# Optimization experiments

Measured on AMD Instinct MI355X. Metric: run time of the kernel, lower is better.

The kernel has to match this reference:

```python
import jax, jax.numpy as jnp
import numpy as np

B, F, V, D_EMB = 16384, 32, 50000, 16
D_IN = F * D_EMB            # 512, concat embedding dim
N_TASK, N_SPEC, N_SH = 2, 2, 2
E = N_TASK * N_SPEC + N_SH  # 6 experts per CGC level
H1, H2 = 512, 256           # expert_params dims
T1, T2 = 128, 64            # tower dims


def setup_inputs() -> dict:
    key = jax.random.key(0)
    ks = iter(jax.random.split(key, 32))
    def w(shape, s=0.05):
        return jax.random.normal(next(ks), shape, jnp.float32) * s
    return dict(
        x_ids=jax.random.randint(next(ks), (B, F), 0, V),
        emb=w((F, V, D_EMB)),
        e1_W1=w((E, D_IN, H1)), e1_b1=jnp.zeros((E, H1), jnp.float32),
        e1_W2=w((E, H1, H2)), e1_b2=jnp.zeros((E, H2), jnp.float32),
        g1_Ws=w((N_TASK, D_IN, N_SPEC + N_SH)), g1_bs=jnp.zeros((N_TASK, N_SPEC + N_SH), jnp.float32),
        g1_Wsh=w((D_IN, E)), g1_bsh=jnp.zeros((E,), jnp.float32),
        e2_W1=w((E, H2, H1)), e2_b1=jnp.zeros((E, H1), jnp.float32),
        e2_W2=w((E, H1, H2)), e2_b2=jnp.zeros((E, H2), jnp.float32),
        g2_Ws=w((N_TASK, H2, N_SPEC + N_SH)), g2_bs=jnp.zeros((N_TASK, N_SPEC + N_SH), jnp.float32),
        tw_W1=w((N_TASK, H2, T1)), tw_b1=jnp.zeros((N_TASK, T1), jnp.float32),
        tw_W2=w((N_TASK, T1, T2)), tw_b2=jnp.zeros((N_TASK, T2), jnp.float32),
    )


def _cgc(x_list, W1, b1, W2, b2, Wg, bg, Wg_sh=None, bg_sh=None):
    # Stack expert inputs: task-t specific experts read x_list[t], shared read x_list[-1].
    X = jnp.stack([x_list[0]] * N_SPEC + [x_list[1]] * N_SPEC + [x_list[-1]] * N_SH)  # [E,B,Din]
    # Grouped two-layer expert MLP (BatchNorm is identity at eval-mode init).
    h = jax.nn.relu(jnp.einsum('ebd,edh->ebh', X, W1) + b1[:, None, :])   # [E,B,H1]
    out = jax.nn.relu(jnp.einsum('ebh,eho->ebo', h, W2) + b2[:, None, :])  # [E,B,H2]
    outs = []
    for t in range(N_TASK):
        gate = jax.nn.softmax(x_list[t] @ Wg[t] + bg[t], axis=-1)          # [B, N_SPEC+N_SH]
        sel = jnp.concatenate([out[t * N_SPEC:(t + 1) * N_SPEC], out[-N_SH:]], axis=0)
        outs.append(jnp.einsum('bk,kbo->bo', gate, sel))
    if Wg_sh is not None:  # shared gate only for levels < n_level
        gate = jax.nn.softmax(x_list[-1] @ Wg_sh + bg_sh, axis=-1)          # [B,E]
        outs.append(jnp.einsum('bk,kbo->bo', gate, out))
    return outs


def reference(x_ids, emb, e1_W1, e1_b1, e1_W2, e1_b2, g1_Ws, g1_bs, g1_Wsh, g1_bsh,
              e2_W1, e2_b1, e2_W2, e2_b2, g2_Ws, g2_bs, tw_W1, tw_b1, tw_W2, tw_b2):
    # Embedding lookup per sparse feature, then flatten (squeeze_dim=True).
    embed_x = emb[jnp.arange(F)[None, :], x_ids].reshape(B, D_IN)  # [B, 512]
    xs = [embed_x] * (N_TASK + 1)
    xs = _cgc(xs, e1_W1, e1_b1, e1_W2, e1_b2, g1_Ws, g1_bs, g1_Wsh, g1_bsh)  # level 1 -> 3 outs
    xs = _cgc(xs, e2_W1, e2_b1, e2_W2, e2_b2, g2_Ws, g2_bs)                  # level 2 -> 2 outs
    ys = []
    for t in range(N_TASK):
        h = jax.nn.relu(xs[t] @ tw_W1[t] + tw_b1[t])
        h = jax.nn.relu(h @ tw_W2[t] + tw_b2[t])
        ys.append(jax.nn.sigmoid(h))  # PredictionLayer('classification')
    return jnp.concatenate(ys, axis=1)  # [B, N_TASK*T2]
```

## Files before the change

### kernel.cpp

```cpp
#include <hip/hip_runtime.h>

typedef unsigned short u16;
typedef __attribute__((ext_vector_type(4))) unsigned short u16x4;
typedef __attribute__((ext_vector_type(8))) unsigned short u16x8;
typedef __attribute__((ext_vector_type(8))) short s16x8;
typedef __attribute__((ext_vector_type(4))) float f32x4;

#define BATCH 16384
#define NFEAT 32
#define NVOCAB 50000

__device__ __forceinline__ u16 f2bf(float f) {
    union { float f; unsigned u; } v; v.f = f;
    unsigned u = v.u;
    return (u16)((u + 0x7fffu + ((u >> 16) & 1u)) >> 16);
}
__device__ __forceinline__ float bf2f(u16 h) {
    union { unsigned u; float f; } v; v.u = ((unsigned)h) << 16;
    return v.f;
}

__device__ __forceinline__ void load_lds16(const u16* g, u16* l) {
    __builtin_amdgcn_global_load_lds(
        (const __attribute__((address_space(1))) void*)g,
        (__attribute__((address_space(3))) void*)l, 16, 0, 0);
}

struct PrepDesc { const float* src; u16* dst; int K; int N; int nz; int zbase; };
struct PrepArgs { PrepDesc d[6]; };

__global__ void prep_weights(PrepArgs args) {
    int z = blockIdx.z;
    int di = 0;
    #pragma unroll
    for (int i = 0; i < 6; i++)
        if (z >= args.d[i].zbase && z < args.d[i].zbase + args.d[i].nz) di = i;
    PrepDesc d = args.d[di];
    int zz = z - d.zbase;
    int k0 = blockIdx.x * 32, n0 = blockIdx.y * 32;
    if (k0 >= d.K || n0 >= d.N) return;
    __shared__ float tile[32][33];
    const float* src = d.src + (long)zz * d.K * d.N;
    u16* dst = d.dst + (long)zz * d.K * d.N;
    int tx = threadIdx.x & 31, ty = threadIdx.x >> 5;
    for (int r = ty; r < 32; r += 8) {
        int k = k0 + r, n = n0 + tx;
        tile[r][tx] = (k < d.K && n < d.N) ? src[(long)k * d.N + n] : 0.f;
    }
    __syncthreads();
    for (int r = ty; r < 32; r += 8) {
        int n = n0 + r, k = k0 + tx;
        if (n < d.N && k < d.K) dst[(long)n * d.K + k] = f2bf(tile[tx][r]);
    }
}

__global__ void gather_embed(const int* __restrict__ ids,
                             const float* __restrict__ emb,
                             u16* __restrict__ out) {
    int idx = blockIdx.x * 256 + threadIdx.x;
    int d4 = idx & 3;
    int f  = (idx >> 2) & 31;
    int b  = idx >> 7;
    int id = ids[b * NFEAT + f];
    const float4* p = (const float4*)(emb + ((long)f * NVOCAB + id) * 16) + d4;
    float4 v = *p;
    u16x4 o;
    o.x = f2bf(v.x); o.y = f2bf(v.y); o.z = f2bf(v.z); o.w = f2bf(v.w);
    *(u16x4*)(out + (long)b * 512 + f * 16 + d4 * 4) = o;
}

struct FusedP {
    const u16* A; const u16* W1t; const float* b1;
    const u16* W2t; const float* b2; u16* O;
    int K1, a_zshift; long a_zstride;
};

__device__ __forceinline__ void expert_impl(const FusedP p) {
    __shared__ u16 sA[64 * 64];
    __shared__ u16 sW[256 * 64];
    __shared__ u16 sH[64 * 128];
    const int z = blockIdx.z;
    const int m0 = blockIdx.x * 64;
    const u16* Ab  = p.A + (long)(z >> p.a_zshift) * p.a_zstride;
    const u16* W1b = p.W1t + (long)z * 512 * p.K1;
    const u16* W2b = p.W2t + (long)z * 256 * 512;
    const int K1 = p.K1;
    const int tid = threadIdx.x;
    const int lane = tid & 63;
    const int w = tid >> 6;
    const int l16 = lane & 15;
    const int q = lane >> 4;
    const int key = l16 & 7;

    const int tr = tid >> 3;
    const int lc = (tid & 7) ^ (tr & 7);
    const u16* gA0 = Ab + (long)(m0 + tr) * K1 + lc * 8;
    const int ldst = (tid & ~63) * 8;

    f32x4 acc[4][4] = {};

    #pragma unroll
    for (int c = 0; c < 4; c++) {
        f32x4 acc1[4][2] = {};
        for (int k0 = 0; k0 < K1; k0 += 64) {
            __syncthreads();
            #pragma unroll
            for (int i = 0; i < 2; i++)
                load_lds16(gA0 + (long)(32 * i) * K1 + k0, &sA[i * 2048 + ldst]);
            #pragma unroll
            for (int i = 0; i < 4; i++)
                load_lds16(W1b + (long)(c * 128 + 32 * i + tr) * K1 + k0 + lc * 8,
                           &sW[i * 2048 + ldst]);
            __syncthreads();
            #pragma unroll
            for (int kk = 0; kk < 2; kk++) {
                const int pc = ((kk << 2) | q) ^ key;
                s16x8 af[4], bf[2];
                #pragma unroll
                for (int mt = 0; mt < 4; mt++)
                    af[mt] = *(const s16x8*)(&sA[(mt * 16 + l16) * 64 + pc * 8]);
                #pragma unroll
                for (int nt = 0; nt < 2; nt++)
                    bf[nt] = *(const s16x8*)(&sW[(w * 32 + nt * 16 + l16) * 64 + pc * 8]);
                #pragma unroll
                for (int mt = 0; mt < 4; mt++)
                    #pragma unroll
                    for (int nt = 0; nt < 2; nt++)
                        acc1[mt][nt] = __builtin_amdgcn_mfma_f32_16x16x32_bf16(
                            bf[nt], af[mt], acc1[mt][nt], 0, 0, 0);
            }
        }
        __syncthreads();
        {
            const float* bb1 = p.b1 + (long)z * 512 + c * 128;
            #pragma unroll
            for (int mt = 0; mt < 4; mt++) {
                int r = mt * 16 + l16;
                #pragma unroll
                for (int nt = 0; nt < 2; nt++) {
                    int col = w * 32 + nt * 16 + q * 4;
                    float4 bv = *(const float4*)(bb1 + col);
                    f32x4 v = acc1[mt][nt];
                    u16x4 o;
                    o.x = f2bf(fmaxf(v.x + bv.x, 0.f));
                    o.y = f2bf(fmaxf(v.y + bv.y, 0.f));
                    o.z = f2bf(fmaxf(v.z + bv.z, 0.f));
                    o.w = f2bf(fmaxf(v.w + bv.w, 0.f));
                    int c8 = col >> 3;
                    *(u16x4*)(&sH[r * 128 + ((c8 ^ (r & 7)) << 3) + (q & 1) * 4]) = o;
                }
            }
        }
        #pragma unroll
        for (int s = 0; s < 2; s++) {
            __syncthreads();
            #pragma unroll
            for (int i = 0; i < 8; i++)
                load_lds16(W2b + (long)(32 * i + tr) * 512 + c * 128 + s * 64 + lc * 8,
                           &sW[i * 2048 + ldst]);
            __syncthreads();
            #pragma unroll
            for (int kk = 0; kk < 2; kk++) {
                const int kg = s * 8 + ((kk << 2) | q);
                const int pc = ((kk << 2) | q) ^ key;
                s16x8 af[4], bf[4];
                #pragma unroll
                for (int mt = 0; mt < 4; mt++) {
                    int r = mt * 16 + l16;
                    af[mt] = *(const s16x8*)(&sH[r * 128 + ((kg ^ key) << 3)]);
                }
                #pragma unroll
                for (int nt = 0; nt < 4; nt++)
                    bf[nt] = *(const s16x8*)(&sW[(w * 64 + nt * 16 + l16) * 64 + pc * 8]);
                #pragma unroll
                for (int mt = 0; mt < 4; mt++)
                    #pragma unroll
                    for (int nt = 0; nt < 4; nt++)
                        acc[mt][nt] = __builtin_amdgcn_mfma_f32_16x16x32_bf16(
                            bf[nt], af[mt], acc[mt][nt], 0, 0, 0);
            }
        }
    }

    const float* bb2 = p.b2 + (long)z * 256;
    u16* Op = p.O + (long)z * BATCH * 256;
    #pragma unroll
    for (int mt = 0; mt < 4; mt++) {
        int grow = m0 + mt * 16 + l16;
        u16* rowp = Op + (long)grow * 256;
        #pragma unroll
        for (int nt = 0; nt < 4; nt++) {
            int gc = w * 64 + nt * 16 + q * 4;
            float4 bv = *(const float4*)(bb2 + gc);
            f32x4 v = acc[mt][nt];
            v.x = fmaxf(v.x + bv.x, 0.f);
            v.y = fmaxf(v.y + bv.y, 0.f);
            v.z = fmaxf(v.z + bv.z, 0.f);
            v.w = fmaxf(v.w + bv.w, 0.f);
            u16x4 o;
            o.x = f2bf(v.x); o.y = f2bf(v.y); o.z = f2bf(v.z); o.w = f2bf(v.w);
            *(u16x4*)(rowp + gc) = o;
        }
    }
}

__global__ __launch_bounds__(256, 2) void fused_l1(FusedP p) { expert_impl(p); }
__global__ __launch_bounds__(256, 2) void fused_l2(FusedP p) { expert_impl(p); }

__global__ __launch_bounds__(256, 1)
void tower_fused(const u16* __restrict__ x2, const u16* __restrict__ W1t,
                 const float* __restrict__ b1, const u16* __restrict__ W2t,
                 const float* __restrict__ b2, float* __restrict__ out) {
    const int t = blockIdx.y, m0 = blockIdx.x * 64;
    __shared__ u16 sX[64 * 256];
    __shared__ u16 sW1[128 * 256];
    __shared__ u16 sH[64 * 136];
    __shared__ u16 sW2[64 * 128];
    __shared__ float sB1[128];
    __shared__ float sB2[64];
    const int tid = threadIdx.x, lane = tid & 63, w = tid >> 6;
    const int l16 = lane & 15, q = lane >> 4;

    #pragma unroll
    for (int i = 0; i < 8; i++) {
        int c = i * 256 + tid, row = c >> 5, kc = c & 31;
        int lcc = (kc & ~7) | ((kc & 7) ^ (row & 7));
        load_lds16(x2 + ((long)t * BATCH + m0 + row) * 256 + lcc * 8,
                   &sX[(i * 256 + (tid & ~63)) * 8]);
    }
    #pragma unroll
    for (int i = 0; i < 16; i++) {
        int c = i * 256 + tid, row = c >> 5, kc = c & 31;
        int lcc = (kc & ~7) | ((kc & 7) ^ (row & 7));
        load_lds16(W1t + ((long)t * 128 + row) * 256 + lcc * 8,
                   &sW1[(i * 256 + (tid & ~63)) * 8]);
    }
    #pragma unroll
    for (int i = 0; i < 4; i++) {
        int c = i * 256 + tid, row = c >> 4, kc = c & 15;
        int lcc = (kc & ~7) | ((kc & 7) ^ (row & 7));
        load_lds16(W2t + ((long)t * 64 + row) * 128 + lcc * 8,
                   &sW2[(i * 256 + (tid & ~63)) * 8]);
    }
    if (tid < 128) sB1[tid] = b1[t * 128 + tid];
    if (tid < 64)  sB2[tid] = b2[t * 64 + tid];
    __syncthreads();

    f32x4 acc1[4][2] = {};
    #pragma unroll
    for (int kk = 0; kk < 8; kk++) {
        int pcb = kk * 4 + q;
        s16x8 af[4], bf[2];
        #pragma unroll
        for (int mt = 0; mt < 4; mt++) {
            int row = mt * 16 + l16;
            int sc = (pcb & ~7) | ((pcb & 7) ^ (row & 7));
            af[mt] = *(const s16x8*)(&sX[row * 256 + sc * 8]);
        }
        #pragma unroll
        for (int nt = 0; nt < 2; nt++) {
            int row = w * 32 + nt * 16 + l16;
            int sc = (pcb & ~7) | ((pcb & 7) ^ (row & 7));
            bf[nt] = *(const s16x8*)(&sW1[row * 256 + sc * 8]);
        }
        #pragma unroll
        for (int mt = 0; mt < 4; mt++)
            #pragma unroll
            for (int nt = 0; nt < 2; nt++)
                acc1[mt][nt] = __builtin_amdgcn_mfma_f32_16x16x32_bf16(
                    bf[nt], af[mt], acc1[mt][nt], 0, 0, 0);
    }
    #pragma unroll
    for (int mt = 0; mt < 4; mt++) {
        int row = mt * 16 + l16;
        #pragma unroll
        for (int nt = 0; nt < 2; nt++) {
            int col = w * 32 + nt * 16 + q * 4;
            f32x4 v = acc1[mt][nt];
            u16x4 o;
            o.x = f2bf(fmaxf(v.x + sB1[col + 0], 0.f));
            o.y = f2bf(fmaxf(v.y + sB1[col + 1], 0.f));
            o.z = f2bf(fmaxf(v.z + sB1[col + 2], 0.f));
            o.w = f2bf(fmaxf(v.w + sB1[col + 3], 0.f));
            *(u16x4*)(&sH[row * 136 + col]) = o;
        }
    }
    __syncthreads();

    f32x4 acc2[4] = {};
    #pragma unroll
    for (int kk = 0; kk < 4; kk++) {
        s16x8 af[4], bf;
        #pragma unroll
        for (int mt = 0; mt < 4; mt++) {
            int row = mt * 16 + l16;
            af[mt] = *(const s16x8*)(&sH[row * 136 + kk * 32 + q * 8]);
        }
        {
            int row = w * 16 + l16;
            int pc = kk * 4 + q;
            int sc = (pc & ~7) | ((pc & 7) ^ (row & 7));
            bf = *(const s16x8*)(&sW2[row * 128 + sc * 8]);
        }
        #pragma unroll
        for (int mt = 0; mt < 4; mt++)
            acc2[mt] = __builtin_amdgcn_mfma_f32_16x16x32_bf16(
                bf, af[mt], acc2[mt], 0, 0, 0);
    }
    #pragma unroll
    for (int mt = 0; mt < 4; mt++) {
        int grow = m0 + mt * 16 + l16;
        int col = w * 16 + q * 4;
        float4 bv = *(const float4*)(sB2 + col);
        f32x4 v = acc2[mt];
        float4 r;
        r.x = 1.f / (1.f + __expf(-(v.x + bv.x)));
        r.y = 1.f / (1.f + __expf(-(v.y + bv.y)));
        r.z = 1.f / (1.f + __expf(-(v.z + bv.z)));
        r.w = 1.f / (1.f + __expf(-(v.w + bv.w)));
        *(float4*)(out + (long)grow * 128 + t * 64 + col) = r;
    }
}

__global__ __launch_bounds__(256)
void gate1(const u16* __restrict__ embed, const u16* __restrict__ out1,
           const float* __restrict__ g1Ws, const float* __restrict__ g1bs,
           const float* __restrict__ gWsh, const float* __restrict__ gbsh,
           u16* __restrict__ x1) {
    const int m0 = blockIdx.x * 8;
    __shared__ float sg[8][16];
    const int tid = threadIdx.x;
    const int row = tid >> 5, l = tid & 31;
    const long rb = m0 + row;

    float a[4] = {0,0,0,0}, b[4] = {0,0,0,0}, c[6] = {0,0,0,0,0,0};
    {
        const u16* er = embed + rb * 512 + l * 16;
        u16x8 xa = *(const u16x8*)(er);
        u16x8 xb = *(const u16x8*)(er + 8);
        #pragma unroll
        for (int u = 0; u < 16; u++) {
            int k = l * 16 + u;
            float xv = bf2f(u < 8 ? xa[u] : xb[u - 8]);
            float4 wa = *(const float4*)(g1Ws + k * 4);
            float4 wb = *(const float4*)(g1Ws + 2048 + k * 4);
            a[0] += xv * wa.x; a[1] += xv * wa.y; a[2] += xv * wa.z; a[3] += xv * wa.w;
            b[0] += xv * wb.x; b[1] += xv * wb.y; b[2] += xv * wb.z; b[3] += xv * wb.w;
            float2 w0 = *(const float2*)(gWsh + k * 6);
            float2 w1 = *(const float2*)(gWsh + k * 6 + 2);
            float2 w2 = *(const float2*)(gWsh + k * 6 + 4);
            c[0] += xv * w0.x; c[1] += xv * w0.y;
            c[2] += xv * w1.x; c[3] += xv * w1.y;
            c[4] += xv * w2.x; c[5] += xv * w2.y;
        }
    }
    #pragma unroll
    for (int off = 1; off < 32; off <<= 1) {
        #pragma unroll
        for (int g = 0; g < 4; g++) { a[g] += __shfl_xor(a[g], off); b[g] += __shfl_xor(b[g], off); }
        #pragma unroll
        for (int g = 0; g < 6; g++) c[g] += __shfl_xor(c[g], off);
    }
    if (l == 0) {
        float mx, s, e[6];
        mx = -1e30f;
        for (int g = 0; g < 4; g++) { a[g] += g1bs[g]; mx = fmaxf(mx, a[g]); }
        s = 0.f; for (int g = 0; g < 4; g++) { e[g] = __expf(a[g] - mx); s += e[g]; }
        for (int g = 0; g < 4; g++) sg[row][g] = e[g] / s;
        mx = -1e30f;
        for (int g = 0; g < 4; g++) { b[g] += g1bs[4 + g]; mx = fmaxf(mx, b[g]); }
        s = 0.f; for (int g = 0; g < 4; g++) { e[g] = __expf(b[g] - mx); s += e[g]; }
        for (int g = 0; g < 4; g++) sg[row][4 + g] = e[g] / s;
        mx = -1e30f;
        for (int g = 0; g < 6; g++) { c[g] += gbsh[g]; mx = fmaxf(mx, c[g]); }
        s = 0.f; for (int g = 0; g < 6; g++) { e[g] = __expf(c[g] - mx); s += e[g]; }
        for (int g = 0; g < 6; g++) sg[row][8 + g] = e[g] / s;
    }
    __syncthreads();

    const int c8 = l * 8;
    const u16* ob = out1 + rb * 256 + c8;
    u16x8 o[6];
    #pragma unroll
    for (int k = 0; k < 6; k++) o[k] = *(const u16x8*)(ob + (long)k * BATCH * 256);
    const float* g = sg[row];
    u16x8 r0, r1, r2;
    #pragma unroll
    for (int u = 0; u < 8; u++) {
        float o0 = bf2f(o[0][u]), o1 = bf2f(o[1][u]), o2 = bf2f(o[2][u]);
        float o3 = bf2f(o[3][u]), o4 = bf2f(o[4][u]), o5 = bf2f(o[5][u]);
        r0[u] = f2bf(g[0] * o0 + g[1] * o1 + g[2] * o4 + g[3] * o5);
        r1[u] = f2bf(g[4] * o2 + g[5] * o3 + g[6] * o4 + g[7] * o5);
        r2[u] = f2bf(g[8] * o0 + g[9] * o1 + g[10] * o2 + g[11] * o3 + g[12] * o4 + g[13] * o5);
    }
    *(u16x8*)(x1 + ((long)0 * BATCH + rb) * 256 + c8) = r0;
    *(u16x8*)(x1 + ((long)1 * BATCH + rb) * 256 + c8) = r1;
    *(u16x8*)(x1 + ((long)2 * BATCH + rb) * 256 + c8) = r2;
}

__global__ __launch_bounds__(256)
void gate2(const u16* __restrict__ x1, const u16* __restrict__ out2,
           const float* __restrict__ g2Ws, const float* __restrict__ g2bs,
           u16* __restrict__ x2) {
    const int m0 = blockIdx.x * 8;
    __shared__ float sg[8][8];
    const int tid = threadIdx.x;
    const int row = tid >> 5, l = tid & 31;
    const long rb = m0 + row;

    float a[4] = {0,0,0,0}, b[4] = {0,0,0,0};
    {
        const u16* e0 = x1 + rb * 256 + l * 8;
        const u16* e1 = e0 + (long)BATCH * 256;
        u16x8 x0 = *(const u16x8*)e0;
        u16x8 x1v = *(const u16x8*)e1;
        #pragma unroll
        for (int u = 0; u < 8; u++) {
            int k = l * 8 + u;
            float4 wa = *(const float4*)(g2Ws + k * 4);
            float4 wb = *(const float4*)(g2Ws + 1024 + k * 4);
            float xv0 = bf2f(x0[u]), xv1 = bf2f(x1v[u]);
            a[0] += xv0 * wa.x; a[1] += xv0 * wa.y; a[2] += xv0 * wa.z; a[3] += xv0 * wa.w;
            b[0] += xv1 * wb.x; b[1] += xv1 * wb.y; b[2] += xv1 * wb.z; b[3] += xv1 * wb.w;
        }
    }
    #pragma unroll
    for (int off = 1; off < 32; off <<= 1) {
        #pragma unroll
        for (int g = 0; g < 4; g++) { a[g] += __shfl_xor(a[g], off); b[g] += __shfl_xor(b[g], off); }
    }
    if (l == 0) {
        float mx, s, e[4];
        mx = -1e30f;
        for (int g = 0; g < 4; g++) { a[g] += g2bs[g]; mx = fmaxf(mx, a[g]); }
        s = 0.f; for (int g = 0; g < 4; g++) { e[g] = __expf(a[g] - mx); s += e[g]; }
        for (int g = 0; g < 4; g++) sg[row][g] = e[g] / s;
        mx = -1e30f;
        for (int g = 0; g < 4; g++) { b[g] += g2bs[4 + g]; mx = fmaxf(mx, b[g]); }
        s = 0.f; for (int g = 0; g < 4; g++) { e[g] = __expf(b[g] - mx); s += e[g]; }
        for (int g = 0; g < 4; g++) sg[row][4 + g] = e[g] / s;
    }
    __syncthreads();

    const int c8 = l * 8;
    const u16* ob = out2 + rb * 256 + c8;
    u16x8 o[6];
    #pragma unroll
    for (int k = 0; k < 6; k++) o[k] = *(const u16x8*)(ob + (long)k * BATCH * 256);
    const float* g = sg[row];
    u16x8 r0, r1;
    #pragma unroll
    for (int u = 0; u < 8; u++) {
        float o0 = bf2f(o[0][u]), o1 = bf2f(o[1][u]), o2 = bf2f(o[2][u]);
        float o3 = bf2f(o[3][u]), o4 = bf2f(o[4][u]), o5 = bf2f(o[5][u]);
        r0[u] = f2bf(g[0] * o0 + g[1] * o1 + g[2] * o4 + g[3] * o5);
        r1[u] = f2bf(g[4] * o2 + g[5] * o3 + g[6] * o4 + g[7] * o5);
    }
    *(u16x8*)(x2 + ((long)0 * BATCH + rb) * 256 + c8) = r0;
    *(u16x8*)(x2 + ((long)1 * BATCH + rb) * 256 + c8) = r1;
}

extern "C" void kernel_launch(void* const* d_in, const int* in_sizes, int n_in,
                              void* d_out, int out_size, void* d_ws, size_t ws_size,
                              hipStream_t stream) {
    const int*   x_ids = (const int*)  d_in[0];
    const float* emb   = (const float*)d_in[1];
    const float* e1W1  = (const float*)d_in[2];
    const float* e1b1  = (const float*)d_in[3];
    const float* e1W2  = (const float*)d_in[4];
    const float* e1b2  = (const float*)d_in[5];
    const float* g1Ws  = (const float*)d_in[6];
    const float* g1bs  = (const float*)d_in[7];
    const float* g1Wsh = (const float*)d_in[8];
    const float* g1bsh = (const float*)d_in[9];
    const float* e2W1  = (const float*)d_in[10];
    const float* e2b1  = (const float*)d_in[11];
    const float* e2W2  = (const float*)d_in[12];
    const float* e2b2  = (const float*)d_in[13];
    const float* g2Ws  = (const float*)d_in[14];
    const float* g2bs  = (const float*)d_in[15];
    const float* twW1  = (const float*)d_in[16];
    const float* twb1  = (const float*)d_in[17];
    const float* twW2  = (const float*)d_in[18];
    const float* twb2  = (const float*)d_in[19];
    float* out = (float*)d_out;

    char* ws = (char*)d_ws;
    u16* embed   = (u16*)(ws + 0);
    u16* wt_e1W1 = (u16*)(ws + 16777216);
    u16* wt_e1W2 = (u16*)(ws + 19922944);
    u16* wt_e2W1 = (u16*)(ws + 21495808);
    u16* wt_e2W2 = (u16*)(ws + 23068672);
    u16* wt_twW1 = (u16*)(ws + 24641536);
    u16* wt_twW2 = (u16*)(ws + 24772608);
    u16* o_buf   = (u16*)(ws + 125468672);
    u16* x1      = (u16*)(ws + 175800320);
    u16* x2      = (u16*)(ws + 200966144);

    PrepArgs pa;
    pa.d[0] = { e1W1, wt_e1W1, 512, 512, 6,  0 };
    pa.d[1] = { e1W2, wt_e1W2, 512, 256, 6,  6 };
    pa.d[2] = { e2W1, wt_e2W1, 256, 512, 6, 12 };
    pa.d[3] = { e2W2, wt_e2W2, 512, 256, 6, 18 };
    pa.d[4] = { twW1, wt_twW1, 256, 128, 2, 24 };
    pa.d[5] = { twW2, wt_twW2, 128,  64, 2, 26 };
    prep_weights<<<dim3(16, 16, 28), 256, 0, stream>>>(pa);

    gather_embed<<<dim3(BATCH * NFEAT * 4 / 256), 256, 0, stream>>>(x_ids, emb, embed);

    FusedP f1 = { embed, wt_e1W1, e1b1, wt_e1W2, e1b2, o_buf, 512, 3, 0L };
    fused_l1<<<dim3(BATCH / 64, 1, 6), 256, 0, stream>>>(f1);

    gate1<<<dim3(BATCH / 8), 256, 0, stream>>>(embed, o_buf, g1Ws, g1bs, g1Wsh, g1bsh, x1);

    FusedP f2 = { x1, wt_e2W1, e2b1, wt_e2W2, e2b2, o_buf, 256, 1, (long)BATCH * 256 };
    fused_l2<<<dim3(BATCH / 64, 1, 6), 256, 0, stream>>>(f2);

    gate2<<<dim3(BATCH / 8), 256, 0, stream>>>(x1, o_buf, g2Ws, g2bs, x2);

    tower_fused<<<dim3(BATCH / 64, 2), 256, 0, stream>>>(x2, wt_twW1, twb1, wt_twW2, twb2, out);
}
```

Measured before the change: 507.2 us.

## Fuse gating and expert mixing into per-level expert megakernels

Replaces the per-expert fused MLP kernels and the separate gate kernels with one kernel per CGC level. Each block now takes 32 rows and loops over all 6 experts, computing the gate softmax up front and accumulating the gated mixture in registers. This removes the round trip of the [6,B,256] expert outputs through global memory and two kernel launches. In exchange the M-tile shrinks from 64 to 32 rows and grid parallelism drops to 512 blocks, so expert weights are reloaded more often per row and MFMA reuse per block is lower.

```diff
diff --git a/kernel.cpp b/kernel.cpp
--- a/kernel.cpp
+++ b/kernel.cpp
@@ -69,22 +69,20 @@
     *(u16x4*)(out + (long)b * 512 + f * 16 + d4 * 4) = o;
 }
 
-struct FusedP {
-    const u16* A; const u16* W1t; const float* b1;
-    const u16* W2t; const float* b2; u16* O;
-    int K1, a_zshift; long a_zstride;
+struct MegaP1 {
+    const u16* A; const u16* W1; const u16* W2;
+    const float* b1; const float* b2;
+    const float* gWs; const float* gbs; const float* gWsh; const float* gbsh;
+    u16* x1;
 };
 
-__device__ __forceinline__ void expert_impl(const FusedP p) {
-    __shared__ u16 sA[64 * 64];
-    __shared__ u16 sW[256 * 64];
-    __shared__ u16 sH[64 * 128];
-    const int z = blockIdx.z;
-    const int m0 = blockIdx.x * 64;
-    const u16* Ab  = p.A + (long)(z >> p.a_zshift) * p.a_zstride;
-    const u16* W1b = p.W1t + (long)z * 512 * p.K1;
-    const u16* W2b = p.W2t + (long)z * 256 * 512;
-    const int K1 = p.K1;
+__global__ __launch_bounds__(256, 2)
+void mega_l1(MegaP1 p) {
+    __shared__ u16 sA[2048];
+    __shared__ u16 sW[16384];
+    __shared__ u16 sH[8192];
+    __shared__ float sg[32][17];
+    const int m0 = blockIdx.x * 32;
     const int tid = threadIdx.x;
     const int lane = tid & 63;
     const int w = tid >> 6;
@@ -92,120 +90,377 @@
     const int q = lane >> 4;
     const int key = l16 & 7;
 
+    {
+        const int row = tid >> 3, l8 = tid & 7;
+        const long rb = m0 + row;
+        float a[4] = {0,0,0,0}, b[4] = {0,0,0,0}, c[6] = {0,0,0,0,0,0};
+        const u16* er = p.A + rb * 512 + l8 * 64;
+        #pragma unroll
+        for (int v = 0; v < 8; v++) {
+            u16x8 xv8 = *(const u16x8*)(er + v * 8);
+            #pragma unroll
+            for (int u = 0; u < 8; u++) {
+                int k = l8 * 64 + v * 8 + u;
+                float xv = bf2f(xv8[u]);
+                float4 wa = *(const float4*)(p.gWs + k * 4);
+                float4 wb = *(const float4*)(p.gWs + 2048 + k * 4);
+                a[0] += xv * wa.x; a[1] += xv * wa.y; a[2] += xv * wa.z; a[3] += xv * wa.w;
+                b[0] += xv * wb.x; b[1] += xv * wb.y; b[2] += xv * wb.z; b[3] += xv * wb.w;
+                float2 w0 = *(const float2*)(p.gWsh + k * 6);
+                float2 w1 = *(const float2*)(p.gWsh + k * 6 + 2);
+                float2 w2 = *(const float2*)(p.gWsh + k * 6 + 4);
+                c[0] += xv * w0.x; c[1] += xv * w0.y;
+                c[2] += xv * w1.x; c[3] += xv * w1.y;
+                c[4] += xv * w2.x; c[5] += xv * w2.y;
+            }
+        }
+        #pragma unroll
+        for (int off = 1; off < 8; off <<= 1) {
+            #pragma unroll
+            for (int g = 0; g < 4; g++) { a[g] += __shfl_xor(a[g], off); b[g] += __shfl_xor(b[g], off); }
+            #pragma unroll
+            for (int g = 0; g < 6; g++) c[g] += __shfl_xor(c[g], off);
+        }
+        if (l8 == 0) {
+            float mx, s, e[6];
+            mx = -1e30f;
+            for (int g = 0; g < 4; g++) { a[g] += p.gbs[g]; mx = fmaxf(mx, a[g]); }
+            s = 0.f; for (int g = 0; g < 4; g++) { e[g] = __expf(a[g] - mx); s += e[g]; }
+            for (int g = 0; g < 4; g++) sg[row][g] = e[g] / s;
+            mx = -1e30f;
+            for (int g = 0; g < 4; g++) { b[g] += p.gbs[4 + g]; mx = fmaxf(mx, b[g]); }
+            s = 0.f; for (int g = 0; g < 4; g++) { e[g] = __expf(b[g] - mx); s += e[g]; }
+            for (int g = 0; g < 4; g++) sg[row][4 + g] = e[g] / s;
+            mx = -1e30f;
+            for (int g = 0; g < 6; g++) { c[g] += p.gbsh[g]; mx = fmaxf(mx, c[g]); }
+            s = 0.f; for (int g = 0; g < 6; g++) { e[g] = __expf(c[g] - mx); s += e[g]; }
+            for (int g = 0; g < 6; g++) sg[row][8 + g] = e[g] / s;
+        }
+    }
+    __syncthreads();
+
     const int tr = tid >> 3;
     const int lc = (tid & 7) ^ (tr & 7);
-    const u16* gA0 = Ab + (long)(m0 + tr) * K1 + lc * 8;
+    const u16* gA = p.A + (long)(m0 + tr) * 512 + lc * 8;
     const int ldst = (tid & ~63) * 8;
 
-    f32x4 acc[4][4] = {};
-
-    #pragma unroll
-    for (int c = 0; c < 4; c++) {
-        f32x4 acc1[4][2] = {};
-        for (int k0 = 0; k0 < K1; k0 += 64) {
+    f32x4 comb0[2][4] = {}, comb1[2][4] = {}, combs[2][4] = {};
+
+    for (int z = 0; z < 6; ++z) {
+        const u16* W1b = p.W1 + (long)z * 512 * 512;
+        const u16* W2b = p.W2 + (long)z * 256 * 512;
+        f32x4 acc[2][4] = {};
+        #pragma unroll
+        for (int c = 0; c < 2; ++c) {
+            f32x4 acc1[2][4] = {};
+            for (int kt = 0; kt < 8; ++kt) {
+                __syncthreads();
+                load_lds16(gA + kt * 64, &sA[ldst]);
+                #pragma unroll
+                for (int i = 0; i < 8; i++)
+                    load_lds16(W1b + (long)(c * 256 + 32 * i + tr) * 512 + kt * 64 + lc * 8,
+                               &sW[i * 2048 + ldst]);
+                __syncthreads();
+                #pragma unroll
+                for (int kk = 0; kk < 2; ++kk) {
+                    const int pc = ((kk << 2) | q) ^ key;
+                    s16x8 af[2], bf[4];
+                    #pragma unroll
+                    for (int mt = 0; mt < 2; ++mt)
+                        af[mt] = *(const s16x8*)(&sA[(mt * 16 + l16) * 64 + pc * 8]);
+                    #pragma unroll
+                    for (int nt = 0; nt < 4; ++nt)
+                        bf[nt] = *(const s16x8*)(&sW[(w * 64 + nt * 16 + l16) * 64 + pc * 8]);
+                    #pragma unroll
+                    for (int mt = 0; mt < 2; ++mt)
+                        #pragma unroll
+                        for (int nt = 0; nt < 4; ++nt)
+                            acc1[mt][nt] = __builtin_amdgcn_mfma_f32_16x16x32_bf16(
+                                bf[nt], af[mt], acc1[mt][nt], 0, 0, 0);
+                }
+            }
             __syncthreads();
-            #pragma unroll
-            for (int i = 0; i < 2; i++)
-                load_lds16(gA0 + (long)(32 * i) * K1 + k0, &sA[i * 2048 + ldst]);
-            #pragma unroll
-            for (int i = 0; i < 4; i++)
-                load_lds16(W1b + (long)(c * 128 + 32 * i + tr) * K1 + k0 + lc * 8,
-                           &sW[i * 2048 + ldst]);
+            {
+                const float* bb1 = p.b1 + (long)z * 512 + c * 256;
+                #pragma unroll
+                for (int mt = 0; mt < 2; ++mt) {
+                    int r = mt * 16 + l16;
+                    #pragma unroll
+                    for (int nt = 0; nt < 4; ++nt) {
+                        int col = w * 64 + nt * 16 + q * 4;
+                        float4 bv = *(const float4*)(bb1 + col);
+                        f32x4 v = acc1[mt][nt];
+                        u16x4 o;
+                        o.x = f2bf(fmaxf(v.x + bv.x, 0.f));
+                        o.y = f2bf(fmaxf(v.y + bv.y, 0.f));
+                        o.z = f2bf(fmaxf(v.z + bv.z, 0.f));
+                        o.w = f2bf(fmaxf(v.w + bv.w, 0.f));
+                        int grp = col >> 3;
+                        *(u16x4*)(&sH[r * 256 + ((grp ^ (r & 7)) << 3) + (q & 1) * 4]) = o;
+                    }
+                }
+            }
+            #pragma unroll
+            for (int s = 0; s < 4; ++s) {
+                __syncthreads();
+                #pragma unroll
+                for (int i = 0; i < 8; i++)
+                    load_lds16(W2b + (long)(32 * i + tr) * 512 + c * 256 + s * 64 + lc * 8,
+                               &sW[i * 2048 + ldst]);
+                __syncthreads();
+                #pragma unroll
+                for (int kk = 0; kk < 2; ++kk) {
+                    const int pc = ((kk << 2) | q) ^ key;
+                    const int kg = s * 8 + ((kk << 2) | q);
+                    s16x8 af[2], bf[4];
+                    #pragma unroll
+                    for (int mt = 0; mt < 2; ++mt) {
+                        int r = mt * 16 + l16;
+                        af[mt] = *(const s16x8*)(&sH[r * 256 + ((kg ^ key) << 3)]);
+                    }
+                    #pragma unroll
+                    for (int nt = 0; nt < 4; ++nt)
+                        bf[nt] = *(const s16x8*)(&sW[(w * 64 + nt * 16 + l16) * 64 + pc * 8]);
+                    #pragma unroll
+                    for (int mt = 0; mt < 2; ++mt)
+                        #pragma unroll
+                        for (int nt = 0; nt < 4; ++nt)
+                            acc[mt][nt] = __builtin_amdgcn_mfma_f32_16x16x32_bf16(
+                                bf[nt], af[mt], acc[mt][nt], 0, 0, 0);
+                }
+            }
+        }
+        #pragma unroll
+        for (int mt = 0; mt < 2; ++mt) {
+            int r = mt * 16 + l16;
+            const float* g = sg[r];
+            float c0 = (z == 0) ? g[0] : (z == 1) ? g[1] : (z == 4) ? g[2] : (z == 5) ? g[3] : 0.f;
+            float c1 = (z == 2) ? g[4] : (z == 3) ? g[5] : (z == 4) ? g[6] : (z == 5) ? g[7] : 0.f;
+            float cs = g[8 + z];
+            #pragma unroll
+            for (int nt = 0; nt < 4; ++nt) {
+                int gc = w * 64 + nt * 16 + q * 4;
+                float4 bv = *(const float4*)(p.b2 + (long)z * 256 + gc);
+                f32x4 v = acc[mt][nt];
+                v.x = fmaxf(v.x + bv.x, 0.f);
+                v.y = fmaxf(v.y + bv.y, 0.f);
+                v.z = fmaxf(v.z + bv.z, 0.f);
+                v.w = fmaxf(v.w + bv.w, 0.f);
+                comb0[mt][nt] += v * c0;
+                comb1[mt][nt] += v * c1;
+                combs[mt][nt] += v * cs;
+            }
+        }
+    }
+
+    #pragma unroll
+    for (int mt = 0; mt < 2; ++mt) {
+        long grow = m0 + mt * 16 + l16;
+        #pragma unroll
+        for (int nt = 0; nt < 4; ++nt) {
+            int gc = w * 64 + nt * 16 + q * 4;
+            u16x4 o;
+            f32x4 v = comb0[mt][nt];
+            o.x = f2bf(v.x); o.y = f2bf(v.y); o.z = f2bf(v.z); o.w = f2bf(v.w);
+            *(u16x4*)(p.x1 + ((long)0 * BATCH + grow) * 256 + gc) = o;
+            v = comb1[mt][nt];
+            o.x = f2bf(v.x); o.y = f2bf(v.y); o.z = f2bf(v.z); o.w = f2bf(v.w);
+            *(u16x4*)(p.x1 + ((long)1 * BATCH + grow) * 256 + gc) = o;
+            v = combs[mt][nt];
+            o.x = f2bf(v.x); o.y = f2bf(v.y); o.z = f2bf(v.z); o.w = f2bf(v.w);
+            *(u16x4*)(p.x1 + ((long)2 * BATCH + grow) * 256 + gc) = o;
+        }
+    }
+}
+
+struct MegaP2 {
+    const u16* x1; const u16* W1; const u16* W2;
+    const float* b1; const float* b2;
+    const float* gWs; const float* gbs;
+    u16* x2;
+};
+
+__global__ __launch_bounds__(256, 2)
+void mega_l2(MegaP2 p) {
+    __shared__ u16 sA[2048];
+    __shared__ u16 sW[16384];
+    __shared__ u16 sH[8192];
+    __shared__ float sg[32][17];
+    const int m0 = blockIdx.x * 32;
+    const int tid = threadIdx.x;
+    const int lane = tid & 63;
+    const int w = tid >> 6;
+    const int l16 = lane & 15;
+    const int q = lane >> 4;
+    const int key = l16 & 7;
+
+    {
+        const int row = tid >> 3, l8 = tid & 7;
+        const long rb = m0 + row;
+        float a[4] = {0,0,0,0}, b[4] = {0,0,0,0};
+        const u16* e0 = p.x1 + rb * 256 + l8 * 32;
+        const u16* e1 = e0 + (long)BATCH * 256;
+        #pragma unroll
+        for (int v = 0; v < 4; v++) {
+            u16x8 x0 = *(const u16x8*)(e0 + v * 8);
+            u16x8 x1v = *(const u16x8*)(e1 + v * 8);
+            #pragma unroll
+            for (int u = 0; u < 8; u++) {
+                int k = l8 * 32 + v * 8 + u;
+                float4 wa = *(const float4*)(p.gWs + k * 4);
+                float4 wb = *(const float4*)(p.gWs + 1024 + k * 4);
+                float xv0 = bf2f(x0[u]), xv1 = bf2f(x1v[u]);
+                a[0] += xv0 * wa.x; a[1] += xv0 * wa.y; a[2] += xv0 * wa.z; a[3] += xv0 * wa.w;
+                b[0] += xv1 * wb.x; b[1] += xv1 * wb.y; b[2] += xv1 * wb.z; b[3] += xv1 * wb.w;
+            }
+        }
+        #pragma unroll
+        for (int off = 1; off < 8; off <<= 1) {
+            #pragma unroll
+            for (int g = 0; g < 4; g++) { a[g] += __shfl_xor(a[g], off); b[g] += __shfl_xor(b[g], off); }
+        }
+        if (l8 == 0) {
+            float mx, s, e[4];
+            mx = -1e30f;
+            for (int g = 0; g < 4; g++) { a[g] += p.gbs[g]; mx = fmaxf(mx, a[g]); }
+            s = 0.f; for (int g = 0; g < 4; g++) { e[g] = __expf(a[g] - mx); s += e[g]; }
+            for (int g = 0; g < 4; g++) sg[row][g] = e[g] / s;
+            mx = -1e30f;
+            for (int g = 0; g < 4; g++) { b[g] += p.gbs[4 + g]; mx = fmaxf(mx, b[g]); }
+            s = 0.f; for (int g = 0; g < 4; g++) { e[g] = __expf(b[g] - mx); s += e[g]; }
+            for (int g = 0; g < 4; g++) sg[row][4 + g] = e[g] / s;
+        }
+    }
+    __syncthreads();
+
+    const int tr = tid >> 3;
+    const int lc = (tid & 7) ^ (tr & 7);
+    const int ldst = (tid & ~63) * 8;
+
+    f32x4 comb0[2][4] = {}, comb1[2][4] = {};
+
+    for (int z = 0; z < 6; ++z) {
+        const u16* gA = p.x1 + ((long)(z >> 1) * BATCH + m0 + tr) * 256 + lc * 8;
+        const u16* W1b = p.W1 + (long)z * 512 * 256;
+        const u16* W2b = p.W2 + (long)z * 256 * 512;
+        f32x4 acc[2][4] = {};
+        #pragma unroll
+        for (int c = 0; c < 2; ++c) {
+            f32x4 acc1[2][4] = {};
+            for (int kt = 0; kt < 4; ++kt) {
+                __syncthreads();
+                load_lds16(gA + kt * 64, &sA[ldst]);
+                #pragma unroll
+                for (int i = 0; i < 8; i++)
+                    load_lds16(W1b + (long)(c * 256 + 32 * i + tr) * 256 + kt * 64 + lc * 8,
+                               &sW[i * 2048 + ldst]);
+                __syncthreads();
+                #pragma unroll
+                for (int kk = 0; kk < 2; ++kk) {
+                    const int pc = ((kk << 2) | q) ^ key;
+                    s16x8 af[2], bf[4];
+                    #pragma unroll
+                    for (int mt = 0; mt < 2; ++mt)
+                        af[mt] = *(const s16x8*)(&sA[(mt * 16 + l16) * 64 + pc * 8]);
+                    #pragma unroll
+                    for (int nt = 0; nt < 4; ++nt)
+                        bf[nt] = *(const s16x8*)(&sW[(w * 64 + nt * 16 + l16) * 64 + pc * 8]);
+                    #pragma unroll
+                    for (int mt = 0; mt < 2; ++mt)
+                        #pragma unroll
+                        for (int nt = 0; nt < 4; ++nt)
+                            acc1[mt][nt] = __builtin_amdgcn_mfma_f32_16x16x32_bf16(
+                                bf[nt], af[mt], acc1[mt][nt], 0, 0, 0);
+                }
+            }
             __syncthreads();
-            #pragma unroll
-            for (int kk = 0; kk < 2; kk++) {
-                const int pc = ((kk << 2) | q) ^ key;
-                s16x8 af[4], bf[2];
-                #pragma unroll
-                for (int mt = 0; mt < 4; mt++)
-                    af[mt] = *(const s16x8*)(&sA[(mt * 16 + l16) * 64 + pc * 8]);
-                #pragma unroll
-                for (int nt = 0; nt < 2; nt++)
-                    bf[nt] = *(const s16x8*)(&sW[(w * 32 + nt * 16 + l16) * 64 + pc * 8]);
-                #pragma unroll
-                for (int mt = 0; mt < 4; mt++)
-                    #pragma unroll
-                    for (int nt = 0; nt < 2; nt++)
-                        acc1[mt][nt] = __builtin_amdgcn_mfma_f32_16x16x32_bf16(
-                            bf[nt], af[mt], acc1[mt][nt], 0, 0, 0);
-            }
-        }
-        __syncthreads();
-        {
-            const float* bb1 = p.b1 + (long)z * 512 + c * 128;
-            #pragma unroll
-            for (int mt = 0; mt < 4; mt++) {
-                int r = mt * 16 + l16;
-                #pragma unroll
-                for (int nt = 0; nt < 2; nt++) {
-                    int col = w * 32 + nt * 16 + q * 4;
-                    float4 bv = *(const float4*)(bb1 + col);
-                    f32x4 v = acc1[mt][nt];
-                    u16x4 o;
-                    o.x = f2bf(fmaxf(v.x + bv.x, 0.f));
-                    o.y = f2bf(fmaxf(v.y + bv.y, 0.f));
-                    o.z = f2bf(fmaxf(v.z + bv.z, 0.f));
-                    o.w = f2bf(fmaxf(v.w + bv.w, 0.f));
-                    int c8 = col >> 3;
-                    *(u16x4*)(&sH[r * 128 + ((c8 ^ (r & 7)) << 3) + (q & 1) * 4]) = o;
+            {
+                const float* bb1 = p.b1 + (long)z * 512 + c * 256;
+                #pragma unroll
+                for (int mt = 0; mt < 2; ++mt) {
+                    int r = mt * 16 + l16;
+                    #pragma unroll
+                    for (int nt = 0; nt < 4; ++nt) {
+                        int col = w * 64 + nt * 16 + q * 4;
+                        float4 bv = *(const float4*)(bb1 + col);
+                        f32x4 v = acc1[mt][nt];
+                        u16x4 o;
+                        o.x = f2bf(fmaxf(v.x + bv.x, 0.f));
+                        o.y = f2bf(fmaxf(v.y + bv.y, 0.f));
+                        o.z = f2bf(fmaxf(v.z + bv.z, 0.f));
+                        o.w = f2bf(fmaxf(v.w + bv.w, 0.f));
+                        int grp = col >> 3;
+                        *(u16x4*)(&sH[r * 256 + ((grp ^ (r & 7)) << 3) + (q & 1) * 4]) = o;
+                    }
                 }
             }
-        }
-        #pragma unroll
-        for (int s = 0; s < 2; s++) {
-            __syncthreads();
-            #pragma unroll
-            for (int i = 0; i < 8; i++)
-                load_lds16(W2b + (long)(32 * i + tr) * 512 + c * 128 + s * 64 + lc * 8,
-                           &sW[i * 2048 + ldst]);
-            __syncthreads();
-            #pragma unroll
-            for (int kk = 0; kk < 2; kk++) {
-                const int kg = s * 8 + ((kk << 2) | q);
-                const int pc = ((kk << 2) | q) ^ key;
-                s16x8 af[4], bf[4];
-                #pragma unroll
-                for (int mt = 0; mt < 4; mt++) {
-                    int r = mt * 16 + l16;
-                    af[mt] = *(const s16x8*)(&sH[r * 128 + ((kg ^ key) << 3)]);
+            #pragma unroll
+            for (int s = 0; s < 4; ++s) {
+                __syncthreads();
+                #pragma unroll
+                for (int i = 0; i < 8; i++)
+                    load_lds16(W2b + (long)(32 * i + tr) * 512 + c * 256 + s * 64 + lc * 8,
+                               &sW[i * 2048 + ldst]);
+                __syncthreads();
+                #pragma unroll
+                for (int kk = 0; kk < 2; ++kk) {
+                    const int pc = ((kk << 2) | q) ^ key;
+                    const int kg = s * 8 + ((kk << 2) | q);
+                    s16x8 af[2], bf[4];
+                    #pragma unroll
+                    for (int mt = 0; mt < 2; ++mt) {
+                        int r = mt * 16 + l16;
+                        af[mt] = *(const s16x8*)(&sH[r * 256 + ((kg ^ key) << 3)]);
+                    }
+                    #pragma unroll
+                    for (int nt = 0; nt < 4; ++nt)
+                        bf[nt] = *(const s16x8*)(&sW[(w * 64 + nt * 16 + l16) * 64 + pc * 8]);
+                    #pragma unroll
+                    for (int mt = 0; mt < 2; ++mt)
+                        #pragma unroll
+                        for (int nt = 0; nt < 4; ++nt)
+                            acc[mt][nt] = __builtin_amdgcn_mfma_f32_16x16x32_bf16(
+                                bf[nt], af[mt], acc[mt][nt], 0, 0, 0);
                 }
-                #pragma unroll
-                for (int nt = 0; nt < 4; nt++)
-                    bf[nt] = *(const s16x8*)(&sW[(w * 64 + nt * 16 + l16) * 64 + pc * 8]);
-                #pragma unroll
-                for (int mt = 0; mt < 4; mt++)
-                    #pragma unroll
-                    for (int nt = 0; nt < 4; nt++)
-                        acc[mt][nt] = __builtin_amdgcn_mfma_f32_16x16x32_bf16(
-                            bf[nt], af[mt], acc[mt][nt], 0, 0, 0);
-            }
-        }
-    }
-
-    const float* bb2 = p.b2 + (long)z * 256;
-    u16* Op = p.O + (long)z * BATCH * 256;
-    #pragma unroll
-    for (int mt = 0; mt < 4; mt++) {
-        int grow = m0 + mt * 16 + l16;
-        u16* rowp = Op + (long)grow * 256;
-        #pragma unroll
-        for (int nt = 0; nt < 4; nt++) {
+            }
+        }
+        #pragma unroll
+        for (int mt = 0; mt < 2; ++mt) {
+            int r = mt * 16 + l16;
+            const float* g = sg[r];
+            float c0 = (z == 0) ? g[0] : (z == 1) ? g[1] : (z == 4) ? g[2] : (z == 5) ? g[3] : 0.f;
+            float c1 = (z == 2) ? g[4] : (z == 3) ? g[5] : (z == 4) ? g[6] : (z == 5) ? g[7] : 0.f;
+            #pragma unroll
+            for (int nt = 0; nt < 4; ++nt) {
+                int gc = w * 64 + nt * 16 + q * 4;
+                float4 bv = *(const float4*)(p.b2 + (long)z * 256 + gc);
+                f32x4 v = acc[mt][nt];
+                v.x = fmaxf(v.x + bv.x, 0.f);
+                v.y = fmaxf(v.y + bv.y, 0.f);
+                v.z = fmaxf(v.z + bv.z, 0.f);
+                v.w = fmaxf(v.w + bv.w, 0.f);
+                comb0[mt][nt] += v * c0;
+                comb1[mt][nt] += v * c1;
+            }
+        }
+    }
+
+    #pragma unroll
+    for (int mt = 0; mt < 2; ++mt) {
+        long grow = m0 + mt * 16 + l16;
+        #pragma unroll
+        for (int nt = 0; nt < 4; ++nt) {
             int gc = w * 64 + nt * 16 + q * 4;
-            float4 bv = *(const float4*)(bb2 + gc);
-            f32x4 v = acc[mt][nt];
-            v.x = fmaxf(v.x + bv.x, 0.f);
-            v.y = fmaxf(v.y + bv.y, 0.f);
-            v.z = fmaxf(v.z + bv.z, 0.f);
-            v.w = fmaxf(v.w + bv.w, 0.f);
             u16x4 o;
+            f32x4 v = comb0[mt][nt];
             o.x = f2bf(v.x); o.y = f2bf(v.y); o.z = f2bf(v.z); o.w = f2bf(v.w);
-            *(u16x4*)(rowp + gc) = o;
-        }
-    }
-}
-
-__global__ __launch_bounds__(256, 2) void fused_l1(FusedP p) { expert_impl(p); }
-__global__ __launch_bounds__(256, 2) void fused_l2(FusedP p) { expert_impl(p); }
+            *(u16x4*)(p.x2 + ((long)0 * BATCH + grow) * 256 + gc) = o;
+            v = comb1[mt][nt];
+            o.x = f2bf(v.x); o.y = f2bf(v.y); o.z = f2bf(v.z); o.w = f2bf(v.w);
+            *(u16x4*)(p.x2 + ((long)1 * BATCH + grow) * 256 + gc) = o;
+        }
+    }
+}
 
 __global__ __launch_bounds__(256, 1)
 void tower_fused(const u16* __restrict__ x2, const u16* __restrict__ W1t,
@@ -320,144 +575,6 @@
         r.w = 1.f / (1.f + __expf(-(v.w + bv.w)));
         *(float4*)(out + (long)grow * 128 + t * 64 + col) = r;
     }
-}
-
-__global__ __launch_bounds__(256)
-void gate1(const u16* __restrict__ embed, const u16* __restrict__ out1,
-           const float* __restrict__ g1Ws, const float* __restrict__ g1bs,
-           const float* __restrict__ gWsh, const float* __restrict__ gbsh,
-           u16* __restrict__ x1) {
-    const int m0 = blockIdx.x * 8;
-    __shared__ float sg[8][16];
-    const int tid = threadIdx.x;
-    const int row = tid >> 5, l = tid & 31;
-    const long rb = m0 + row;
-
-    float a[4] = {0,0,0,0}, b[4] = {0,0,0,0}, c[6] = {0,0,0,0,0,0};
-    {
-        const u16* er = embed + rb * 512 + l * 16;
-        u16x8 xa = *(const u16x8*)(er);
-        u16x8 xb = *(const u16x8*)(er + 8);
-        #pragma unroll
-        for (int u = 0; u < 16; u++) {
-            int k = l * 16 + u;
-            float xv = bf2f(u < 8 ? xa[u] : xb[u - 8]);
-            float4 wa = *(const float4*)(g1Ws + k * 4);
-            float4 wb = *(const float4*)(g1Ws + 2048 + k * 4);
-            a[0] += xv * wa.x; a[1] += xv * wa.y; a[2] += xv * wa.z; a[3] += xv * wa.w;
-            b[0] += xv * wb.x; b[1] += xv * wb.y; b[2] += xv * wb.z; b[3] += xv * wb.w;
-            float2 w0 = *(const float2*)(gWsh + k * 6);
-            float2 w1 = *(const float2*)(gWsh + k * 6 + 2);
-            float2 w2 = *(const float2*)(gWsh + k * 6 + 4);
-            c[0] += xv * w0.x; c[1] += xv * w0.y;
-            c[2] += xv * w1.x; c[3] += xv * w1.y;
-            c[4] += xv * w2.x; c[5] += xv * w2.y;
-        }
-    }
-    #pragma unroll
-    for (int off = 1; off < 32; off <<= 1) {
-        #pragma unroll
-        for (int g = 0; g < 4; g++) { a[g] += __shfl_xor(a[g], off); b[g] += __shfl_xor(b[g], off); }
-        #pragma unroll
-        for (int g = 0; g < 6; g++) c[g] += __shfl_xor(c[g], off);
-    }
-    if (l == 0) {
-        float mx, s, e[6];
-        mx = -1e30f;
-        for (int g = 0; g < 4; g++) { a[g] += g1bs[g]; mx = fmaxf(mx, a[g]); }
-        s = 0.f; for (int g = 0; g < 4; g++) { e[g] = __expf(a[g] - mx); s += e[g]; }
-        for (int g = 0; g < 4; g++) sg[row][g] = e[g] / s;
-        mx = -1e30f;
-        for (int g = 0; g < 4; g++) { b[g] += g1bs[4 + g]; mx = fmaxf(mx, b[g]); }
-        s = 0.f; for (int g = 0; g < 4; g++) { e[g] = __expf(b[g] - mx); s += e[g]; }
-        for (int g = 0; g < 4; g++) sg[row][4 + g] = e[g] / s;
-        mx = -1e30f;
-        for (int g = 0; g < 6; g++) { c[g] += gbsh[g]; mx = fmaxf(mx, c[g]); }
-        s = 0.f; for (int g = 0; g < 6; g++) { e[g] = __expf(c[g] - mx); s += e[g]; }
-        for (int g = 0; g < 6; g++) sg[row][8 + g] = e[g] / s;
-    }
-    __syncthreads();
-
-    const int c8 = l * 8;
-    const u16* ob = out1 + rb * 256 + c8;
-    u16x8 o[6];
-    #pragma unroll
-    for (int k = 0; k < 6; k++) o[k] = *(const u16x8*)(ob + (long)k * BATCH * 256);
-    const float* g = sg[row];
-    u16x8 r0, r1, r2;
-    #pragma unroll
-    for (int u = 0; u < 8; u++) {
-        float o0 = bf2f(o[0][u]), o1 = bf2f(o[1][u]), o2 = bf2f(o[2][u]);
-        float o3 = bf2f(o[3][u]), o4 = bf2f(o[4][u]), o5 = bf2f(o[5][u]);
-        r0[u] = f2bf(g[0] * o0 + g[1] * o1 + g[2] * o4 + g[3] * o5);
-        r1[u] = f2bf(g[4] * o2 + g[5] * o3 + g[6] * o4 + g[7] * o5);
-        r2[u] = f2bf(g[8] * o0 + g[9] * o1 + g[10] * o2 + g[11] * o3 + g[12] * o4 + g[13] * o5);
-    }
-    *(u16x8*)(x1 + ((long)0 * BATCH + rb) * 256 + c8) = r0;
-    *(u16x8*)(x1 + ((long)1 * BATCH + rb) * 256 + c8) = r1;
-    *(u16x8*)(x1 + ((long)2 * BATCH + rb) * 256 + c8) = r2;
-}
-
-__global__ __launch_bounds__(256)
-void gate2(const u16* __restrict__ x1, const u16* __restrict__ out2,
-           const float* __restrict__ g2Ws, const float* __restrict__ g2bs,
-           u16* __restrict__ x2) {
-    const int m0 = blockIdx.x * 8;
-    __shared__ float sg[8][8];
-    const int tid = threadIdx.x;
-    const int row = tid >> 5, l = tid & 31;
-    const long rb = m0 + row;
-
-    float a[4] = {0,0,0,0}, b[4] = {0,0,0,0};
-    {
-        const u16* e0 = x1 + rb * 256 + l * 8;
-        const u16* e1 = e0 + (long)BATCH * 256;
-        u16x8 x0 = *(const u16x8*)e0;
-        u16x8 x1v = *(const u16x8*)e1;
-        #pragma unroll
-        for (int u = 0; u < 8; u++) {
-            int k = l * 8 + u;
-            float4 wa = *(const float4*)(g2Ws + k * 4);
-            float4 wb = *(const float4*)(g2Ws + 1024 + k * 4);
-            float xv0 = bf2f(x0[u]), xv1 = bf2f(x1v[u]);
-            a[0] += xv0 * wa.x; a[1] += xv0 * wa.y; a[2] += xv0 * wa.z; a[3] += xv0 * wa.w;
-            b[0] += xv1 * wb.x; b[1] += xv1 * wb.y; b[2] += xv1 * wb.z; b[3] += xv1 * wb.w;
-        }
-    }
-    #pragma unroll
-    for (int off = 1; off < 32; off <<= 1) {
-        #pragma unroll
-        for (int g = 0; g < 4; g++) { a[g] += __shfl_xor(a[g], off); b[g] += __shfl_xor(b[g], off); }
-    }
-    if (l == 0) {
-        float mx, s, e[4];
-        mx = -1e30f;
-        for (int g = 0; g < 4; g++) { a[g] += g2bs[g]; mx = fmaxf(mx, a[g]); }
-        s = 0.f; for (int g = 0; g < 4; g++) { e[g] = __expf(a[g] - mx); s += e[g]; }
-        for (int g = 0; g < 4; g++) sg[row][g] = e[g] / s;
-        mx = -1e30f;
-        for (int g = 0; g < 4; g++) { b[g] += g2bs[4 + g]; mx = fmaxf(mx, b[g]); }
-        s = 0.f; for (int g = 0; g < 4; g++) { e[g] = __expf(b[g] - mx); s += e[g]; }
-        for (int g = 0; g < 4; g++) sg[row][4 + g] = e[g] / s;
-    }
-    __syncthreads();
-
-    const int c8 = l * 8;
-    const u16* ob = out2 + rb * 256 + c8;
-    u16x8 o[6];
-    #pragma unroll
-    for (int k = 0; k < 6; k++) o[k] = *(const u16x8*)(ob + (long)k * BATCH * 256);
-    const float* g = sg[row];
-    u16x8 r0, r1;
-    #pragma unroll
-    for (int u = 0; u < 8; u++) {
-        float o0 = bf2f(o[0][u]), o1 = bf2f(o[1][u]), o2 = bf2f(o[2][u]);
-        float o3 = bf2f(o[3][u]), o4 = bf2f(o[4][u]), o5 = bf2f(o[5][u]);
-        r0[u] = f2bf(g[0] * o0 + g[1] * o1 + g[2] * o4 + g[3] * o5);
-        r1[u] = f2bf(g[4] * o2 + g[5] * o3 + g[6] * o4 + g[7] * o5);
-    }
-    *(u16x8*)(x2 + ((long)0 * BATCH + rb) * 256 + c8) = r0;
-    *(u16x8*)(x2 + ((long)1 * BATCH + rb) * 256 + c8) = r1;
 }
 
 extern "C" void kernel_launch(void* const* d_in, const int* in_sizes, int n_in,
@@ -493,7 +610,6 @@
     u16* wt_e2W2 = (u16*)(ws + 23068672);
     u16* wt_twW1 = (u16*)(ws + 24641536);
     u16* wt_twW2 = (u16*)(ws + 24772608);
-    u16* o_buf   = (u16*)(ws + 125468672);
     u16* x1      = (u16*)(ws + 175800320);
     u16* x2      = (u16*)(ws + 200966144);
 
@@ -508,15 +624,11 @@
 
     gather_embed<<<dim3(BATCH * NFEAT * 4 / 256), 256, 0, stream>>>(x_ids, emb, embed);
 
-    FusedP f1 = { embed, wt_e1W1, e1b1, wt_e1W2, e1b2, o_buf, 512, 3, 0L };
-    fused_l1<<<dim3(BATCH / 64, 1, 6), 256, 0, stream>>>(f1);
-
-    gate1<<<dim3(BATCH / 8), 256, 0, stream>>>(embed, o_buf, g1Ws, g1bs, g1Wsh, g1bsh, x1);
-
-    FusedP f2 = { x1, wt_e2W1, e2b1, wt_e2W2, e2b2, o_buf, 256, 1, (long)BATCH * 256 };
-    fused_l2<<<dim3(BATCH / 64, 1, 6), 256, 0, stream>>>(f2);
-
-    gate2<<<dim3(BATCH / 8), 256, 0, stream>>>(x1, o_buf, g2Ws, g2bs, x2);
+    MegaP1 m1 = { embed, wt_e1W1, wt_e1W2, e1b1, e1b2, g1Ws, g1bs, g1Wsh, g1bsh, x1 };
+    mega_l1<<<dim3(BATCH / 32), 256, 0, stream>>>(m1);
+
+    MegaP2 m2 = { x1, wt_e2W1, wt_e2W2, e2b1, e2b2, g2Ws, g2bs, x2 };
+    mega_l2<<<dim3(BATCH / 32), 256, 0, stream>>>(m2);
 
     tower_fused<<<dim3(BATCH / 64, 2), 256, 0, stream>>>(x2, wt_twW1, twb1, wt_twW2, twb2, out);
 }
```

After: 528.3 us. 4.2% more time.
